# Optimization experiments

Measured on AMD Instinct MI355X. Metric: run time of the kernel, lower is better.

Reference implementation:

```python
import jax, jax.numpy as jnp
import numpy as np

N, E, D, H = 50000, 600000, 128, 8
C = D // H  # per-head channels

def _layernorm(x, g, b, eps=1e-5):
    mu = jnp.mean(x, axis=-1, keepdims=True)
    var = jnp.var(x, axis=-1, keepdims=True)
    return (x - mu) * jax.lax.rsqrt(var + eps) * g + b

def setup_inputs() -> dict:
    key = jax.random.key(0)
    ks = jax.random.split(key, 16)
    s = 0.02
    w = lambda k, shape: jax.random.normal(k, shape, jnp.float32) * s
    return {
        "x": jax.random.normal(ks[0], (N, D), jnp.float32),
        "edge_attr": jax.random.normal(ks[1], (E, D), jnp.float32),
        "edge_index": jax.random.randint(ks[2], (2, E), 0, N, jnp.int64),
        # TransformerConv params (PyG: lin_query/key/value with bias, lin_edge no bias, lin_skip root weight)
        "Wq": w(ks[3], (D, D)), "bq": jnp.zeros((D,), jnp.float32),
        "Wk": w(ks[4], (D, D)), "bk": jnp.zeros((D,), jnp.float32),
        "Wv": w(ks[5], (D, D)), "bv": jnp.zeros((D,), jnp.float32),
        "We": w(ks[6], (D, D)),
        "Wskip": w(ks[7], (D, D)), "bskip": jnp.zeros((D,), jnp.float32),
        # FFN
        "W1": w(ks[8], (D, 4 * D)), "b1": jnp.zeros((4 * D,), jnp.float32),
        "W2": w(ks[9], (4 * D, D)), "b2": jnp.zeros((D,), jnp.float32),
        # LayerNorms + residual scale
        "g1": jnp.ones((D,), jnp.float32), "beta1": jnp.zeros((D,), jnp.float32),
        "g2": jnp.ones((D,), jnp.float32), "beta2": jnp.zeros((D,), jnp.float32),
        "alpha": jnp.ones((1,), jnp.float32),
    }

def reference(x, edge_attr, edge_index, Wq, bq, Wk, bk, Wv, bv, We, Wskip, bskip,
              W1, b1, W2, b2, g1, beta1, g2, beta2, alpha):
    n = x.shape[0]
    src, dst = edge_index[0], edge_index[1]

    h = _layernorm(x, g1, beta1)

    # --- TransformerConv ---
    q = (h @ Wq + bq)[dst].reshape(-1, H, C)              # [E,H,C]
    e = (edge_attr @ We).reshape(-1, H, C)                # [E,H,C]
    k = (h @ Wk + bk)[src].reshape(-1, H, C) + e          # [E,H,C]
    v = (h @ Wv + bv)[src].reshape(-1, H, C) + e          # [E,H,C]

    logits = jnp.sum(q * k, axis=-1) / jnp.sqrt(jnp.float32(C))  # [E,H]
    # segment softmax over incoming edges per destination node
    m = jax.ops.segment_max(logits, dst, num_segments=n)          # [N,H]
    p = jnp.exp(logits - m[dst])                                   # [E,H]
    z = jax.ops.segment_sum(p, dst, num_segments=n)               # [N,H]
    attn = p / (z[dst] + 1e-16)                                    # [E,H]

    msg = attn[..., None] * v                                      # [E,H,C]
    out = jax.ops.segment_sum(msg, dst, num_segments=n).reshape(n, H * C)
    out = out + h @ Wskip + bskip                                  # root weight (skip)

    x = x + alpha * out

    h2 = _layernorm(x, g2, beta2)
    ffn = jax.nn.silu(h2 @ W1 + b1) @ W2 + b2
    return x + ffn
```

## Files before the change

kernel.cpp:

```cpp
#include <hip/hip_runtime.h>
#include <hip/hip_bf16.h>

typedef __bf16 bf16x8 __attribute__((ext_vector_type(8)));
typedef __bf16 bf16x4 __attribute__((ext_vector_type(4)));
typedef __bf16 bf16x2 __attribute__((ext_vector_type(2)));
typedef float f32x4 __attribute__((ext_vector_type(4)));
using bf16 = __hip_bfloat16;

__global__ __launch_bounds__(256) void t_k(const float* __restrict__ W,
                                           bf16* __restrict__ WT, int K, int N)
{
    int idx = blockIdx.x * 256 + threadIdx.x;
    if (idx >= K * N) return;
    int n = idx / K, k = idx % K;
    WT[idx] = __float2bfloat16(W[(size_t)k * N + n]);
}

__global__ __launch_bounds__(256) void bcat_k(const float* __restrict__ a, const float* __restrict__ b,
                                              const float* __restrict__ c, const float* __restrict__ d,
                                              float* __restrict__ o)
{
    int i = threadIdx.x + blockIdx.x * 256;
    if (i >= 512) return;
    o[i] = (i < 128) ? a[i] : (i < 256) ? b[i - 128] : (i < 384) ? c[i - 256] : d[i - 384];
}

template <int MODE, bool AF32>
__global__ __launch_bounds__(512) void gemm2_k(
    const void* __restrict__ Av, const bf16* __restrict__ WT,
    const float* __restrict__ bias, void* __restrict__ Cout,
    const float* __restrict__ resid, const int* __restrict__ rowperm,
    int M, int K, int Nout)
{
    __shared__ __bf16 As[128 * 128];
    __shared__ __bf16 Ws[128 * 128];

    const int tid  = threadIdx.x;
    const int wave = tid >> 6;
    const int lane = tid & 63;
    const int row0 = blockIdx.x * 128;
    const int col0 = blockIdx.y * 128;

    f32x4 acc[8];
#pragma unroll
    for (int i = 0; i < 8; i++) acc[i] = (f32x4){0.f, 0.f, 0.f, 0.f};

    for (int k0 = 0; k0 < K; k0 += 128) {
        if constexpr (AF32) {
            const float* A = (const float*)Av;
#pragma unroll
            for (int i = 0; i < 8; i++) {
                int idx = tid + i * 512;
                int r = idx >> 5, c4 = idx & 31;
                bf16x4 o;
                if (row0 + r < M) {
                    f32x4 v = *reinterpret_cast<const f32x4*>(A + (size_t)(row0 + r) * K + k0 + c4 * 4);
#pragma unroll
                    for (int j = 0; j < 4; j++) o[j] = (__bf16)v[j];
                } else {
#pragma unroll
                    for (int j = 0; j < 4; j++) o[j] = (__bf16)0.f;
                }
                int col = (c4 >> 1) ^ (r & 7);
                *reinterpret_cast<bf16x4*>(&As[r * 128 + col * 8 + (c4 & 1) * 4]) = o;
            }
        } else {
            const bf16* A = (const bf16*)Av;
#pragma unroll
            for (int i = 0; i < 4; i++) {
                int idx = tid + i * 512;
                int r = idx >> 4, c = idx & 15;
                bf16x8 v;
                if (row0 + r < M) {
                    v = *reinterpret_cast<const bf16x8*>(A + (size_t)(row0 + r) * K + k0 + c * 8);
                } else {
#pragma unroll
                    for (int j = 0; j < 8; j++) v[j] = (__bf16)0.f;
                }
                *reinterpret_cast<bf16x8*>(&As[r * 128 + ((c ^ (r & 7)) * 8)]) = v;
            }
        }
#pragma unroll
        for (int i = 0; i < 4; i++) {
            int idx = tid + i * 512;
            int r = idx >> 4, c = idx & 15;
            bf16x8 v = *reinterpret_cast<const bf16x8*>(WT + (size_t)(col0 + r) * K + k0 + c * 8);
            *reinterpret_cast<bf16x8*>(&Ws[r * 128 + ((c ^ (r & 7)) * 8)]) = v;
        }
        __syncthreads();

        const int mrow = wave * 16 + (lane & 15);
        const int kq = lane >> 4;
#pragma unroll
        for (int kk = 0; kk < 4; kk++) {
            int cidx = kk * 4 + kq;
            bf16x8 a = *reinterpret_cast<const bf16x8*>(&As[mrow * 128 + ((cidx ^ (mrow & 7)) * 8)]);
#pragma unroll
            for (int ct = 0; ct < 8; ct++) {
                int nrow = ct * 16 + (lane & 15);
                bf16x8 b = *reinterpret_cast<const bf16x8*>(&Ws[nrow * 128 + ((cidx ^ (nrow & 7)) * 8)]);
                acc[ct] = __builtin_amdgcn_mfma_f32_16x16x32_bf16(a, b, acc[ct], 0, 0, 0);
            }
        }
        __syncthreads();
    }

    const int rbase = row0 + wave * 16 + ((lane >> 4) << 2);
    int orow[4];
#pragma unroll
    for (int r = 0; r < 4; r++) {
        int row = rbase + r;
        orow[r] = (row < M) ? (rowperm ? rowperm[row] : row) : -1;
    }
#pragma unroll
    for (int ct = 0; ct < 8; ct++) {
        int col = col0 + ct * 16 + (lane & 15);
        float bv = bias ? bias[col] : 0.f;
#pragma unroll
        for (int r = 0; r < 4; r++) {
            if (orow[r] < 0) continue;
            float v = acc[ct][r] + bv;
            if constexpr (MODE == 2) v = v / (1.f + __expf(-v));
            if constexpr (MODE == 3) v += resid[(size_t)orow[r] * 128 + col];
            if constexpr (MODE == 3) {
                ((float*)Cout)[(size_t)orow[r] * Nout + col] = v;
            } else {
                ((bf16*)Cout)[(size_t)orow[r] * Nout + col] = __float2bfloat16(v);
            }
        }
    }
}

__global__ __launch_bounds__(256) void egemm_k(
    const float* __restrict__ A, const bf16* __restrict__ WT,
    bf16* __restrict__ C, const int* __restrict__ rowperm, int M)
{
    __shared__ __bf16 Ws[128 * 128];
#pragma unroll
    for (int i = 0; i < 8; i++) {
        int idx = threadIdx.x + i * 256;
        int r = idx >> 4, c = idx & 15;
        bf16x8 v = *reinterpret_cast<const bf16x8*>(WT + r * 128 + c * 8);
        *reinterpret_cast<bf16x8*>(&Ws[r * 128 + ((c ^ (r & 7)) * 8)]) = v;
    }
    __syncthreads();

    const int lane = threadIdx.x & 63;
    const int wave = threadIdx.x >> 6;
    const int r16  = lane & 15;
    const int kq   = lane >> 4;
    const int ntiles = (M + 15) >> 4;

    for (int t = blockIdx.x * 4 + wave; t < ntiles; t += gridDim.x * 4) {
        const int row0 = t * 16;
        const int arow = row0 + r16;

        bf16x8 a[4];
        if (arow < M) {
            const float* ap = A + (size_t)arow * 128 + kq * 8;
#pragma unroll
            for (int kk = 0; kk < 4; kk++) {
                f32x4 lo = *reinterpret_cast<const f32x4*>(ap + kk * 32);
                f32x4 hi = *reinterpret_cast<const f32x4*>(ap + kk * 32 + 4);
#pragma unroll
                for (int j = 0; j < 4; j++) {
                    a[kk][j]     = (__bf16)lo[j];
                    a[kk][j + 4] = (__bf16)hi[j];
                }
            }
        } else {
#pragma unroll
            for (int kk = 0; kk < 4; kk++)
#pragma unroll
                for (int j = 0; j < 8; j++) a[kk][j] = (__bf16)0.f;
        }

        f32x4 acc[8];
#pragma unroll
        for (int i = 0; i < 8; i++) acc[i] = (f32x4){0.f, 0.f, 0.f, 0.f};
#pragma unroll
        for (int kk = 0; kk < 4; kk++) {
            int cidx = kk * 4 + kq;
#pragma unroll
            for (int ct = 0; ct < 8; ct++) {
                int nrow = ct * 16 + r16;
                bf16x8 b = *reinterpret_cast<const bf16x8*>(&Ws[nrow * 128 + ((cidx ^ (nrow & 7)) * 8)]);
                acc[ct] = __builtin_amdgcn_mfma_f32_16x16x32_bf16(a[kk], b, acc[ct], 0, 0, 0);
            }
        }

        const int rbase = row0 + (kq << 2);
#pragma unroll
        for (int r = 0; r < 4; r++) {
            int row = rbase + r;
            if (row >= M) continue;
            size_t orow = (size_t)(rowperm ? rowperm[row] : row);
#pragma unroll
            for (int ct = 0; ct < 8; ct++) {
                C[orow * 128 + ct * 16 + r16] = __float2bfloat16(acc[ct][r]);
            }
        }
    }
}

__global__ __launch_bounds__(256) void ln_k(
    const float* __restrict__ x, const float* __restrict__ g,
    const float* __restrict__ beta, bf16* __restrict__ h, int Nrows)
{
    int row = blockIdx.x * 4 + (threadIdx.x >> 6);
    int lane = threadIdx.x & 63;
    if (row >= Nrows) return;
    size_t base = (size_t)row * 128;
    float v0 = x[base + lane], v1 = x[base + lane + 64];
    float s = v0 + v1, ss = v0 * v0 + v1 * v1;
#pragma unroll
    for (int off = 32; off; off >>= 1) {
        s += __shfl_xor(s, off, 64);
        ss += __shfl_xor(ss, off, 64);
    }
    float mu = s * (1.f / 128.f);
    float var = ss * (1.f / 128.f) - mu * mu;
    float rs = rsqrtf(var + 1e-5f);
    h[base + lane]      = __float2bfloat16((v0 - mu) * rs * g[lane] + beta[lane]);
    h[base + lane + 64] = __float2bfloat16((v1 - mu) * rs * g[lane + 64] + beta[lane + 64]);
}

__global__ __launch_bounds__(256) void hist_k(const int* __restrict__ ei, int* __restrict__ cnt, int E)
{
    int e = blockIdx.x * 256 + threadIdx.x;
    if (e < E) atomicAdd(&cnt[ei[E + e]], 1);
}

__global__ __launch_bounds__(1024) void scan_k(const int* __restrict__ cnt, int* __restrict__ offset, int N)
{
    __shared__ int tmp[1024];
    __shared__ int s_running;
    int tid = threadIdx.x;
    if (tid == 0) { s_running = 0; offset[0] = 0; }
    __syncthreads();
    for (int base = 0; base < N; base += 1024) {
        int v = (base + tid < N) ? cnt[base + tid] : 0;
        tmp[tid] = v;
        __syncthreads();
#pragma unroll
        for (int off = 1; off < 1024; off <<= 1) {
            int t = (tid >= off) ? tmp[tid - off] : 0;
            __syncthreads();
            tmp[tid] += t;
            __syncthreads();
        }
        int run = s_running;
        if (base + tid < N) offset[base + tid + 1] = run + tmp[tid];
        __syncthreads();
        if (tid == 0) s_running = run + tmp[1023];
        __syncthreads();
    }
}

__global__ __launch_bounds__(256) void scatter_k(
    const int* __restrict__ ei, const int* __restrict__ offset,
    int* __restrict__ cursor, int* __restrict__ srcs, int* __restrict__ epos, int E)
{
    int e = blockIdx.x * 256 + threadIdx.x;
    if (e >= E) return;
    int src = ei[e];
    int dst = ei[E + e];
    int r = atomicAdd(&cursor[dst], 1);
    int j = offset[dst] + r;
    srcs[j] = src;
    epos[e] = j;
}

__global__ __launch_bounds__(256) void gather_k(
    const int* __restrict__ srcs, const int* __restrict__ offset,
    const bf16* __restrict__ QKVS, const bf16* __restrict__ Ep,
    const float* __restrict__ x, const float* __restrict__ alpha,
    const float* __restrict__ g, const float* __restrict__ beta,
    float* __restrict__ xn, bf16* __restrict__ h2, int N)
{
    int node = blockIdx.x * 4 + (threadIdx.x >> 6);
    if (node >= N) return;
    int lane = threadIdx.x & 63;
    int c = lane * 2;

    bf16x2 qv = *reinterpret_cast<const bf16x2*>(QKVS + (size_t)node * 512 + c);
    float q0 = (float)qv[0], q1 = (float)qv[1];

    int start = offset[node], end = offset[node + 1];
    float den = 0.f, num0 = 0.f, num1 = 0.f;

    bf16x2 kv, vv, ev;
    if (start < end) {
        const bf16* sp = QKVS + (size_t)srcs[start] * 512 + c;
        kv = *reinterpret_cast<const bf16x2*>(sp + 128);
        vv = *reinterpret_cast<const bf16x2*>(sp + 256);
        ev = *reinterpret_cast<const bf16x2*>(Ep + (size_t)start * 128 + c);
    }
    for (int j = start; j < end; j++) {
        bf16x2 kc = kv, vc = vv, ec = ev;
        if (j + 1 < end) {
            const bf16* sp = QKVS + (size_t)srcs[j + 1] * 512 + c;
            kv = *reinterpret_cast<const bf16x2*>(sp + 128);
            vv = *reinterpret_cast<const bf16x2*>(sp + 256);
            ev = *reinterpret_cast<const bf16x2*>(Ep + (size_t)(j + 1) * 128 + c);
        }
        float e0 = (float)ec[0], e1 = (float)ec[1];
        float part = q0 * ((float)kc[0] + e0) + q1 * ((float)kc[1] + e1);
        part += __shfl_xor(part, 1, 64);
        part += __shfl_xor(part, 2, 64);
        part += __shfl_xor(part, 4, 64);
        float p = __expf(part * 0.25f);
        den  += p;
        num0 += p * ((float)vc[0] + e0);
        num1 += p * ((float)vc[1] + e1);
    }

    size_t base = (size_t)node * 128;
    float invz = 1.f / (den + 1e-16f);
    float al = alpha[0];
    float s0 = (float)QKVS[(size_t)node * 512 + 384 + c];
    float s1 = (float)QKVS[(size_t)node * 512 + 384 + c + 1];
    float o0 = num0 * invz + s0;
    float o1 = num1 * invz + s1;
    float x0 = x[base + c] + al * o0;
    float x1 = x[base + c + 1] + al * o1;
    xn[base + c] = x0;
    xn[base + c + 1] = x1;

    float s = x0 + x1, ss = x0 * x0 + x1 * x1;
#pragma unroll
    for (int off = 32; off; off >>= 1) {
        s += __shfl_xor(s, off, 64);
        ss += __shfl_xor(ss, off, 64);
    }
    float mu = s * (1.f / 128.f);
    float var = ss * (1.f / 128.f) - mu * mu;
    float rs = rsqrtf(var + 1e-5f);
    h2[base + c]     = __float2bfloat16((x0 - mu) * rs * g[c] + beta[c]);
    h2[base + c + 1] = __float2bfloat16((x1 - mu) * rs * g[c + 1] + beta[c + 1]);
}

extern "C" void kernel_launch(void* const* d_in, const int* in_sizes, int n_in,
                              void* d_out, int out_size, void* d_ws, size_t ws_size,
                              hipStream_t stream)
{
    const float* x         = (const float*)d_in[0];
    const float* edge_attr = (const float*)d_in[1];
    const int*   ei        = (const int*)d_in[2];
    const float* Wq = (const float*)d_in[3];  const float* bq = (const float*)d_in[4];
    const float* Wk = (const float*)d_in[5];  const float* bk = (const float*)d_in[6];
    const float* Wv = (const float*)d_in[7];  const float* bv = (const float*)d_in[8];
    const float* We = (const float*)d_in[9];
    const float* Wskip = (const float*)d_in[10]; const float* bskip = (const float*)d_in[11];
    const float* W1 = (const float*)d_in[12]; const float* b1 = (const float*)d_in[13];
    const float* W2 = (const float*)d_in[14]; const float* b2 = (const float*)d_in[15];
    const float* g1 = (const float*)d_in[16]; const float* beta1 = (const float*)d_in[17];
    const float* g2 = (const float*)d_in[18]; const float* beta2 = (const float*)d_in[19];
    const float* alpha = (const float*)d_in[20];

    const int N = in_sizes[0] / 128;
    const int E = in_sizes[2] / 2;

    char* w = (char*)d_ws;
    auto alloc = [&](size_t bytes) {
        char* p = w;
        w += (bytes + 255) & ~(size_t)255;
        return p;
    };
    bf16*  h      = (bf16*)alloc((size_t)N * 128 * 2);
    bf16*  QKVS   = (bf16*)alloc((size_t)N * 512 * 2);
    bf16*  Ep     = (bf16*)alloc((size_t)E * 128 * 2);
    float* xn     = (float*)alloc((size_t)N * 128 * 4);
    bf16*  h2     = (bf16*)alloc((size_t)N * 128 * 2);
    bf16*  t      = (bf16*)alloc((size_t)N * 512 * 2);
    int*   cnt    = (int*)alloc((size_t)N * 4);
    int*   cursor = (int*)alloc((size_t)N * 4);
    int*   offset = (int*)alloc((size_t)(N + 1) * 4);
    int*   srcs   = (int*)alloc((size_t)E * 4);
    int*   epos   = (int*)alloc((size_t)E * 4);
    bf16*  WTqkvs = (bf16*)alloc((size_t)512 * 128 * 2);
    bf16*  WTe    = (bf16*)alloc((size_t)128 * 128 * 2);
    bf16*  WT1    = (bf16*)alloc((size_t)512 * 128 * 2);
    bf16*  WT2    = (bf16*)alloc((size_t)128 * 512 * 2);
    float* bqkvs  = (float*)alloc((size_t)512 * 4);

    t_k<<<64, 256, 0, stream>>>(Wq, WTqkvs, 128, 128);
    t_k<<<64, 256, 0, stream>>>(Wk, WTqkvs + 128 * 128, 128, 128);
    t_k<<<64, 256, 0, stream>>>(Wv, WTqkvs + 256 * 128, 128, 128);
    t_k<<<64, 256, 0, stream>>>(Wskip, WTqkvs + 384 * 128, 128, 128);
    t_k<<<64, 256, 0, stream>>>(We, WTe, 128, 128);
    t_k<<<256, 256, 0, stream>>>(W1, WT1, 128, 512);
    t_k<<<256, 256, 0, stream>>>(W2, WT2, 512, 128);
    bcat_k<<<2, 256, 0, stream>>>(bq, bk, bv, bskip, bqkvs);

    hipMemsetAsync(cnt, 0, (size_t)N * 4, stream);
    hipMemsetAsync(cursor, 0, (size_t)N * 4, stream);
    hist_k<<<(E + 255) / 256, 256, 0, stream>>>(ei, cnt, E);
    scan_k<<<1, 1024, 0, stream>>>(cnt, offset, N);
    scatter_k<<<(E + 255) / 256, 256, 0, stream>>>(ei, offset, cursor, srcs, epos, E);

    ln_k<<<(N + 3) / 4, 256, 0, stream>>>(x, g1, beta1, h, N);

    gemm2_k<0, false><<<dim3((N + 127) / 128, 4), 512, 0, stream>>>(h, WTqkvs, bqkvs, QKVS, nullptr, nullptr, N, 128, 512);

    egemm_k<<<1280, 256, 0, stream>>>(edge_attr, WTe, Ep, epos, E);

    gather_k<<<(N + 3) / 4, 256, 0, stream>>>(srcs, offset, QKVS, Ep, x, alpha, g2, beta2, xn, h2, N);

    gemm2_k<2, false><<<dim3((N + 127) / 128, 4), 512, 0, stream>>>(h2, WT1, b1, t, nullptr, nullptr, N, 128, 512);
    gemm2_k<3, false><<<dim3((N + 127) / 128, 1), 512, 0, stream>>>(t, WT2, b2, d_out, xn, nullptr, N, 512, 128);
}
```

Measured before the change: 903.5 us.

## Add persistent K=128 GEMM with LDS-resident swizzled weights; wave-shuffle scan

Adds a persistent GEMM kernel for the K=128 projections (QKV/skip and FFN up with SiLU). Each block loads one 128x128 weight slice into XOR-swizzled LDS once, then each wave loops over 16-row tiles using bf16 MFMA. This is meant to amortize weight loads and launch overhead over many row tiles. The single-block prefix scan is also rewritten to use wave shuffles plus a small per-wave sum array instead of a barrier-heavy Hillis-Steele LDS scan. The costs are lower occupancy from 32KB of LDS per block and direct row-major output stores.

```diff
diff --git a/kernel.cpp b/kernel.cpp
--- a/kernel.cpp
+++ b/kernel.cpp
@@ -203,6 +203,79 @@
     }
 }
 
+template <int MODE>
+__global__ __launch_bounds__(256) void ngemm_k(
+    const bf16* __restrict__ A, const bf16* __restrict__ WT,
+    const float* __restrict__ bias, bf16* __restrict__ C,
+    int M, int Nout)
+{
+    __shared__ __bf16 Ws[128 * 128];
+    const int col0 = blockIdx.y * 128;
+#pragma unroll
+    for (int i = 0; i < 8; i++) {
+        int idx = threadIdx.x + i * 256;
+        int r = idx >> 4, c = idx & 15;
+        bf16x8 v = *reinterpret_cast<const bf16x8*>(WT + (size_t)(col0 + r) * 128 + c * 8);
+        *reinterpret_cast<bf16x8*>(&Ws[r * 128 + ((c ^ (r & 7)) * 8)]) = v;
+    }
+    __syncthreads();
+
+    const int lane = threadIdx.x & 63;
+    const int wave = threadIdx.x >> 6;
+    const int r16  = lane & 15;
+    const int kq   = lane >> 4;
+    const int ntiles = (M + 15) >> 4;
+
+    float bcol[8];
+#pragma unroll
+    for (int ct = 0; ct < 8; ct++) bcol[ct] = bias[col0 + ct * 16 + r16];
+
+    for (int t = blockIdx.x * 4 + wave; t < ntiles; t += gridDim.x * 4) {
+        const int row0 = t * 16;
+        const int arow = row0 + r16;
+
+        bf16x8 a[4];
+        if (arow < M) {
+            const bf16* ap = A + (size_t)arow * 128 + kq * 8;
+#pragma unroll
+            for (int kk = 0; kk < 4; kk++)
+                a[kk] = *reinterpret_cast<const bf16x8*>(ap + kk * 32);
+        } else {
+#pragma unroll
+            for (int kk = 0; kk < 4; kk++)
+#pragma unroll
+                for (int j = 0; j < 8; j++) a[kk][j] = (__bf16)0.f;
+        }
+
+        f32x4 acc[8];
+#pragma unroll
+        for (int i = 0; i < 8; i++) acc[i] = (f32x4){0.f, 0.f, 0.f, 0.f};
+#pragma unroll
+        for (int kk = 0; kk < 4; kk++) {
+            int cidx = kk * 4 + kq;
+#pragma unroll
+            for (int ct = 0; ct < 8; ct++) {
+                int nrow = ct * 16 + r16;
+                bf16x8 b = *reinterpret_cast<const bf16x8*>(&Ws[nrow * 128 + ((cidx ^ (nrow & 7)) * 8)]);
+                acc[ct] = __builtin_amdgcn_mfma_f32_16x16x32_bf16(a[kk], b, acc[ct], 0, 0, 0);
+            }
+        }
+
+        const int rbase = row0 + (kq << 2);
+#pragma unroll
+        for (int r = 0; r < 4; r++) {
+            int row = rbase + r;
+            if (row >= M) continue;
+#pragma unroll
+            for (int ct = 0; ct < 8; ct++) {
+                float v = acc[ct][r] + bcol[ct];
+                if constexpr (MODE == 2) v = v / (1.f + __expf(-v));
+                C[(size_t)row * Nout + col0 + ct * 16 + r16] = __float2bfloat16(v);
+            }
+        }
+    }
+}
+
 __global__ __launch_bounds__(256) void ln_k(
     const float* __restrict__ x, const float* __restrict__ g,
     const float* __restrict__ beta, bf16* __restrict__ h, int Nrows)
@@ -233,26 +306,34 @@
 
 __global__ __launch_bounds__(1024) void scan_k(const int* __restrict__ cnt, int* __restrict__ offset, int N)
 {
-    __shared__ int tmp[1024];
+    __shared__ int wsum[16];
     __shared__ int s_running;
-    int tid = threadIdx.x;
+    int tid  = threadIdx.x;
+    int lane = tid & 63;
+    int wv   = tid >> 6;
     if (tid == 0) { s_running = 0; offset[0] = 0; }
     __syncthreads();
     for (int base = 0; base < N; base += 1024) {
         int v = (base + tid < N) ? cnt[base + tid] : 0;
-        tmp[tid] = v;
-        __syncthreads();
-#pragma unroll
-        for (int off = 1; off < 1024; off <<= 1) {
-            int t = (tid >= off) ? tmp[tid - off] : 0;
-            __syncthreads();
-            tmp[tid] += t;
-            __syncthreads();
-        }
+        int s = v;
+#pragma unroll
+        for (int d = 1; d < 64; d <<= 1) {
+            int t = __shfl_up(s, d, 64);
+            if (lane >= d) s += t;
+        }
+        if (lane == 63) wsum[wv] = s;
+        __syncthreads();
+        if (tid == 0) {
+            int acc = 0;
+#pragma unroll
+            for (int i = 0; i < 16; i++) { acc += wsum[i]; wsum[i] = acc; }
+        }
+        __syncthreads();
         int run = s_running;
-        if (base + tid < N) offset[base + tid + 1] = run + tmp[tid];
-        __syncthreads();
-        if (tid == 0) s_running = run + tmp[1023];
+        int wexcl = (wv > 0) ? wsum[wv - 1] : 0;
+        if (base + tid < N) offset[base + tid + 1] = run + wexcl + s;
+        __syncthreads();
+        if (tid == 0) s_running = run + wsum[15];
         __syncthreads();
     }
 }
@@ -401,12 +482,12 @@
 
     ln_k<<<(N + 3) / 4, 256, 0, stream>>>(x, g1, beta1, h, N);
 
-    gemm2_k<0, false><<<dim3((N + 127) / 128, 4), 512, 0, stream>>>(h, WTqkvs, bqkvs, QKVS, nullptr, nullptr, N, 128, 512);
+    ngemm_k<0><<<dim3(256, 4), 256, 0, stream>>>(h, WTqkvs, bqkvs, QKVS, N, 512);
 
     egemm_k<<<1280, 256, 0, stream>>>(edge_attr, WTe, Ep, epos, E);
 
     gather_k<<<(N + 3) / 4, 256, 0, stream>>>(srcs, offset, QKVS, Ep, x, alpha, g2, beta2, xn, h2, N);
 
-    gemm2_k<2, false><<<dim3((N + 127) / 128, 4), 512, 0, stream>>>(h2, WT1, b1, t, nullptr, nullptr, N, 128, 512);
+    ngemm_k<2><<<dim3(256, 4), 256, 0, stream>>>(h2, WT1, b1, t, N, 512);
     gemm2_k<3, false><<<dim3((N + 127) / 128, 1), 512, 0, stream>>>(t, WT2, b2, d_out, xn, nullptr, N, 512, 128);
 }
```

After: 824.2 us. -8.8%, faster.
